# Optimization experiments

Hardware: AMD Instinct MI355X
Metric: run time of the kernel (lower is better)

## Reference

```python
import jax, jax.numpy as jnp
import numpy as np

NHEADS = 16
DIM = 1024


def setup_inputs() -> dict:
    key = jax.random.key(0)
    k1, k2, k3 = jax.random.split(key, 3)
    B, S, D = 4, 2048, DIM
    x = jax.random.normal(k1, (B, S, D), dtype=jnp.float32)
    W_qkv = jax.random.normal(k2, (D, 3 * D), dtype=jnp.float32) * (1.0 / np.sqrt(D))
    b_qkv = jax.random.normal(k3, (3 * D,), dtype=jnp.float32) * 0.01
    return {"x": x, "W_qkv": W_qkv, "b_qkv": b_qkv}


def reference(x, W_qkv, b_qkv):
    B, S, D = x.shape
    H = NHEADS
    Dh = D // H
    qkv = x @ W_qkv + b_qkv                      # [B, S, 3D]
    q, k, v = jnp.split(qkv, 3, axis=-1)         # each [B, S, D]
    # [B, S, H, Dh] -> [B, H, S, Dh]
    q = q.reshape(B, S, H, Dh).transpose(0, 2, 1, 3)
    k = k.reshape(B, S, H, Dh).transpose(0, 2, 1, 3)
    v = v.reshape(B, S, H, Dh).transpose(0, 2, 1, 3)
    scale = 1.0 / np.sqrt(Dh).astype(np.float32)
    scores = jnp.einsum('bhqd,bhkd->bhqk', q, k) * scale
    attn = jax.nn.softmax(scores, axis=-1)
    out = jnp.einsum('bhqk,bhkd->bhqd', attn, v)  # [B, H, S, Dh]
    # FAITHFUL to original: raw view [B,H,S,Dh] -> [B, S, H*Dh] (no transpose back)
    return out.reshape(B, S, H * Dh)
```

## Files before the change

### kernel.cpp

```cpp
#include <hip/hip_runtime.h>
#include <hip/hip_bf16.h>
#include <stdint.h>

typedef float          f32x4 __attribute__((ext_vector_type(4)));
typedef short          s16x8 __attribute__((ext_vector_type(8)));
typedef short          s16x4 __attribute__((ext_vector_type(4)));
typedef unsigned short u16;
typedef u16            u16x4 __attribute__((ext_vector_type(4)));
typedef u16            u16x8 __attribute__((ext_vector_type(8)));

#define DMODEL 1024
#define NH     16
#define DH     64
#define SEQ    2048
#define BATCH  4
#define NROW   (BATCH*SEQ)
#define N3     (3*DMODEL)

#define KEXP 0.1803368801f

__device__ __forceinline__ u16 f2bf(float f) {
    __hip_bfloat16 h = __float2bfloat16(f);
    u16 u;
    __builtin_memcpy(&u, &h, 2);
    return u;
}

typedef const __attribute__((address_space(1))) void* gas_t;
typedef __attribute__((address_space(3))) void* las_t;
__device__ __forceinline__ void async16(void* lds, const void* g) {
    __builtin_amdgcn_global_load_lds((gas_t)g, (las_t)lds, 16, 0, 0);
}

__device__ __forceinline__ f32x4 mfma16(s16x8 a, s16x8 b, f32x4 c) {
    return __builtin_amdgcn_mfma_f32_16x16x32_bf16(a, b, c, 0, 0, 0);
}

#if !defined(__HIP_DEVICE_COMPILE__)
__device__ __forceinline__ f32x4 mfma16k16(s16x4 a, s16x4 b, f32x4 c) {
    (void)a; (void)b; return c;
}
#elif __has_builtin(__builtin_amdgcn_mfma_f32_16x16x16bf16_1k)
__device__ __forceinline__ f32x4 mfma16k16(s16x4 a, s16x4 b, f32x4 c) {
    return __builtin_amdgcn_mfma_f32_16x16x16bf16_1k(a, b, c, 0, 0, 0);
}
#elif __has_builtin(__builtin_amdgcn_mfma_f32_16x16x16_bf16)
__device__ __forceinline__ f32x4 mfma16k16(s16x4 a, s16x4 b, f32x4 c) {
    return __builtin_amdgcn_mfma_f32_16x16x16_bf16(a, b, c, 0, 0, 0);
}
#else
#error "no 16x16x16 bf16 mfma builtin on device"
#endif

__global__ __launch_bounds__(256)
void cast_fused_kernel(const float* __restrict__ xin, u16* __restrict__ xb,
                       const float* __restrict__ W,  u16* __restrict__ Wt)
{
    __shared__ u16 T[64][72];
    const int t = threadIdx.x;
    if (blockIdx.x < 4096) {
        const int i = blockIdx.x * 256 + t;
        const f32x4* p = (const f32x4*)xin;
        f32x4 a = p[2*i], b = p[2*i+1];
        u16x8 o;
        o[0]=f2bf(a[0]); o[1]=f2bf(a[1]); o[2]=f2bf(a[2]); o[3]=f2bf(a[3]);
        o[4]=f2bf(b[0]); o[5]=f2bf(b[1]); o[6]=f2bf(b[2]); o[7]=f2bf(b[3]);
        ((u16x8*)xb)[i] = o;
        return;
    }
    const int bid2 = blockIdx.x - 4096;
    const int n0 = (bid2 % (N3/64)) * 64;
    const int k0 = (bid2 / (N3/64)) * 64;
    {
        const int c4 = t & 15, rr = t >> 4;
        #pragma unroll
        for (int ri = 0; ri < 4; ++ri) {
            const int r = ri*16 + rr;
            f32x4 v = *(const f32x4*)&W[(size_t)(k0 + r) * N3 + n0 + c4*4];
            #pragma unroll
            for (int e = 0; e < 4; ++e) T[r][c4*4+e] = f2bf(v[e]);
        }
    }
    __syncthreads();
    {
        const int nr = t >> 2, kq = t & 3;
        #pragma unroll
        for (int pp = 0; pp < 2; ++pp) {
            const int kb = kq + pp*4;
            u16x8 o;
            #pragma unroll
            for (int e = 0; e < 8; ++e) o[e] = T[kb*8+e][nr];
            *(u16x8*)&Wt[(size_t)(n0 + nr) * DMODEL + k0 + kb*8] = o;
        }
    }
}

__global__ __launch_bounds__(256)
void qkv_mfma_kernel(const u16* __restrict__ xb, const u16* __restrict__ Wt,
                     const float* __restrict__ bias,
                     u16* __restrict__ Qb, u16* __restrict__ Kb, u16* __restrict__ Vt)
{
    __shared__ u16 As[128*32];
    __shared__ u16 Bs[128*32];

    const int tid  = threadIdx.x;
    const int lane = tid & 63;
    const int w    = tid >> 6;
    const int wm   = w >> 1, wn = w & 1;
    const int n0   = blockIdx.x * 128;
    const int m0   = blockIdx.y * 128;

    const int srow = w*32 + (lane >> 2);
    const int scol = (lane & 3) * 8;
    u16* ad0 = &As[(w*2+0)*512 + lane*8];
    u16* ad1 = &As[(w*2+1)*512 + lane*8];
    u16* bd0 = &Bs[(w*2+0)*512 + lane*8];
    u16* bd1 = &Bs[(w*2+1)*512 + lane*8];
    const u16* ag0 = &xb[(size_t)(m0 + srow)      * DMODEL + scol];
    const u16* ag1 = &xb[(size_t)(m0 + srow + 16) * DMODEL + scol];
    const u16* bg0 = &Wt[(size_t)(n0 + srow)      * DMODEL + scol];
    const u16* bg1 = &Wt[(size_t)(n0 + srow + 16) * DMODEL + scol];

    f32x4 acc[4][4];
    #pragma unroll
    for (int i = 0; i < 4; ++i)
        #pragma unroll
        for (int j = 0; j < 4; ++j)
            acc[i][j] = (f32x4){0.f, 0.f, 0.f, 0.f};

    for (int k0 = 0; k0 < DMODEL; k0 += 32) {
        async16(ad0, ag0 + k0);
        async16(ad1, ag1 + k0);
        async16(bd0, bg0 + k0);
        async16(bd1, bg1 + k0);
        __syncthreads();
        s16x8 af[4], bf[4];
        #pragma unroll
        for (int mi = 0; mi < 4; ++mi)
            af[mi] = *(const s16x8*)&As[(wm*64 + mi*16 + (lane&15))*32 + (lane>>4)*8];
        #pragma unroll
        for (int ni = 0; ni < 4; ++ni)
            bf[ni] = *(const s16x8*)&Bs[(wn*64 + ni*16 + (lane&15))*32 + (lane>>4)*8];
        #pragma unroll
        for (int mi = 0; mi < 4; ++mi)
            #pragma unroll
            for (int ni = 0; ni < 4; ++ni)
                acc[mi][ni] = mfma16(af[mi], bf[ni], acc[mi][ni]);
        __syncthreads();
    }

    const int part  = n0 >> 10;
    const int col_l = lane & 15;
    const int h     = ((n0 & 1023) >> 6) + wn;
    float bv[4];
    #pragma unroll
    for (int ni = 0; ni < 4; ++ni) bv[ni] = bias[n0 + wn*64 + ni*16 + col_l];

    const int rbase = m0 + wm*64 + (lane>>4)*4;
    u16* qk = (part == 0) ? Qb : Kb;
    #pragma unroll
    for (int mi = 0; mi < 4; ++mi) {
        const int r0 = rbase + mi*16;
        const int b  = r0 >> 11;
        const int s  = r0 & 2047;
        #pragma unroll
        for (int ni = 0; ni < 4; ++ni) {
            const int d = ni*16 + col_l;
            if (part < 2) {
                u16* base = &qk[(((size_t)b*NH + h)*SEQ + s)*DH + d];
                #pragma unroll
                for (int j = 0; j < 4; ++j) {
                    float v = acc[mi][ni][j] + bv[ni];
                    if (part == 0) v *= KEXP;
                    base[(size_t)j*DH] = f2bf(v);
                }
            } else {
                u16x4 o;
                #pragma unroll
                for (int j = 0; j < 4; ++j) o[j] = f2bf(acc[mi][ni][j] + bv[ni]);
                *(u16x4*)&Vt[(((size_t)b*NH + h)*DH + d)*SEQ + s] = o;
            }
        }
    }
}

__global__ __launch_bounds__(512)
void attn_mfma_kernel(const u16* __restrict__ Qb, const u16* __restrict__ Kb,
                      const u16* __restrict__ Vt, float* __restrict__ out)
{
    __shared__ u16 Ks[2][2][64*64];
    __shared__ u16 Vs[2][2][64*64];

    const int tid  = threadIdx.x;
    const int lane = tid & 63;
    const int w    = tid >> 6;
    const int q0   = blockIdx.x * 256;
    const int bh   = blockIdx.y;
    const size_t qkoff = (size_t)bh * SEQ * DH;

    const int lrow = lane >> 4;
    const int lcol = lane & 15;

    s16x8 qf[2][2];
    #pragma unroll
    for (int mi = 0; mi < 2; ++mi) {
        const u16* qp = &Qb[qkoff + (size_t)(q0 + w*32 + mi*16 + lcol)*DH + lrow*8];
        qf[mi][0] = *(const s16x8*)(qp);
        qf[mi][1] = *(const s16x8*)(qp + 32);
    }

    const int skey = tid >> 3;
    const int sg   = tid & 7;
    const int gsw8 = (sg ^ (skey & 7)) * 8;
    const int sdo  = tid * 8;
    const u16* kgb = &Kb[qkoff + (size_t)skey * DH + gsw8];
    const u16* vgb = &Vt[((size_t)bh * DH + skey) * SEQ + gsw8];

    f32x4 oacc[2][4];
    #pragma unroll
    for (int mi = 0; mi < 2; ++mi)
        #pragma unroll
        for (int nd = 0; nd < 4; ++nd) oacc[mi][nd] = (f32x4){0.f,0.f,0.f,0.f};
    float psum[2] = {0.f, 0.f};

#define STAGE(buf, kb2) do {                                          \
        const size_t _o = (size_t)(kb2) * 128;                        \
        async16(&Ks[buf][0][sdo], kgb + (_o     ) * DH);              \
        async16(&Ks[buf][1][sdo], kgb + (_o + 64) * DH);              \
        async16(&Vs[buf][0][sdo], vgb + _o);                          \
        async16(&Vs[buf][1][sdo], vgb + _o + 64);                     \
    } while (0)

#define COMPUTE(buf, sub) do {                                                   \
        const char* ksb = (const char*)Ks[buf][sub];                             \
        const char* vsb = (const char*)Vs[buf][sub];                             \
        f32x4 sacc[2][4];                                                        \
        _Pragma("unroll")                                                        \
        for (int mi = 0; mi < 2; ++mi)                                           \
            _Pragma("unroll")                                                    \
            for (int ni = 0; ni < 4; ++ni) sacc[mi][ni] = (f32x4){0.f,0.f,0.f,0.f}; \
        _Pragma("unroll")                                                        \
        for (int ni = 0; ni < 4; ++ni) {                                         \
            const int key  = ni*16 + lcol;                                       \
            const int rowb = key * 128;                                          \
            _Pragma("unroll")                                                    \
            for (int ks = 0; ks < 2; ++ks) {                                     \
                const int cb = (ks*64 + lrow*16) ^ ((key & 7) << 4);             \
                s16x8 kf = *(const s16x8*)(ksb + rowb + cb);                     \
                _Pragma("unroll")                                                \
                for (int mi = 0; mi < 2; ++mi)                                   \
                    sacc[mi][ni] = mfma16(kf, qf[mi][ks], sacc[mi][ni]);         \
            }                                                                    \
        }                                                                        \
                \
        s16x4 pa[2][4];                                                          \
        _Pragma("unroll")                                                        \
        for (int mi = 0; mi < 2; ++mi) {                                         \
            float rs = 0.f;                                                      \
            _Pragma("unroll")                                                    \
            for (int ni = 0; ni < 4; ++ni) {                                     \
                u16x4 pk;                                                        \
                _Pragma("unroll")                                                \
                for (int jj = 0; jj < 4; ++jj) {                                 \
                    const float p = __builtin_amdgcn_exp2f(sacc[mi][ni][jj]);    \
                    rs += p;                                                     \
                    pk[jj] = f2bf(p);                                            \
                }                                                                \
                pa[mi][ni] = (s16x4)pk;                                          \
            }                                                                    \
            psum[mi] += rs;                                                      \
        }                                                                        \
                \
        _Pragma("unroll")                                                        \
        for (int ni = 0; ni < 4; ++ni) {                                         \
            _Pragma("unroll")                                                    \
            for (int nd = 0; nd < 4; ++nd) {                                     \
                const int d    = nd*16 + lcol;                                   \
                const int gran = ni*2 + (lrow >> 1);                             \
                const int vb   = d*128 + ((gran ^ (d & 7)) << 4) + (lrow & 1)*8; \
                s16x4 vf = *(const s16x4*)(vsb + vb);                            \
                _Pragma("unroll")                                                \
                for (int mi = 0; mi < 2; ++mi)                                   \
                    oacc[mi][nd] = mfma16k16(pa[mi][ni], vf, oacc[mi][nd]);      \
            }                                                                    \
        }                                                                        \
    } while (0)

    STAGE(0, 0);
    asm volatile("s_waitcnt vmcnt(0)" ::: "memory");
    __builtin_amdgcn_s_barrier();

    for (int kb2 = 0; kb2 < SEQ/128; kb2 += 2) {
        STAGE(1, kb2 + 1);
        COMPUTE(0, 0);
        COMPUTE(0, 1);
        asm volatile("s_waitcnt vmcnt(0)" ::: "memory");
        __builtin_amdgcn_s_barrier();
        if (kb2 + 2 < SEQ/128) STAGE(0, kb2 + 2);
        COMPUTE(1, 0);
        COMPUTE(1, 1);
        asm volatile("s_waitcnt vmcnt(0)" ::: "memory");
        __builtin_amdgcn_s_barrier();
    }

#undef STAGE
#undef COMPUTE

    float* op = out + qkoff;
    #pragma unroll
    for (int mi = 0; mi < 2; ++mi) {
        float l = psum[mi];
        l += __shfl_xor(l, 16);
        l += __shfl_xor(l, 32);
        #pragma unroll
        for (int jj = 0; jj < 4; ++jj) {
            const float rinv = 1.0f / __shfl(l, lrow*4 + jj);
            const int q = q0 + w*32 + mi*16 + lrow*4 + jj;
            #pragma unroll
            for (int nd = 0; nd < 4; ++nd)
                op[(size_t)q*DH + nd*16 + lcol] = oacc[mi][nd][jj] * rinv;
        }
    }
}

extern "C" void kernel_launch(void* const* d_in, const int* in_sizes, int n_in,
                              void* d_out, int out_size, void* d_ws, size_t ws_size,
                              hipStream_t stream)
{
    const float* x    = (const float*)d_in[0];
    const float* W    = (const float*)d_in[1];
    const float* bias = (const float*)d_in[2];
    float* out = (float*)d_out;

    u16* xb = (u16*)d_ws;
    u16* Wt = xb + (size_t)NROW * DMODEL;
    u16* Qb = Wt + (size_t)N3 * DMODEL;
    u16* Kb = Qb + (size_t)BATCH*NH*SEQ*DH;
    u16* Vt = Kb + (size_t)BATCH*NH*SEQ*DH;

    cast_fused_kernel<<<4096 + 768, 256, 0, stream>>>(x, xb, W, Wt);
    qkv_mfma_kernel<<<dim3(N3/128, NROW/128), 256, 0, stream>>>(xb, Wt, bias, Qb, Kb, Vt);
    attn_mfma_kernel<<<dim3(SEQ/256, BATCH*NH), 512, 0, stream>>>(Qb, Kb, Vt, out);
}
```

Measured before the change: 172.7 us.

## Switch attention kernel to 32x32x16 bf16 MFMA tiles

Rewrites the attention inner loop to use 32x32x16 bf16 MFMA for both QK^T and PV, replacing 16x16x32 and 16x16x16 instructions. Each wave now handles 32 queries as a single M tile, with cross-half lane shuffles to rearrange the exponentiated probabilities into the A-operand layout for the PV product. The aim is fewer MFMA issues and LDS fragment reads per tile and a larger K per instruction. The cost is extra shuffles per block, larger accumulator register tiles, and a new output-store mapping.

Measured after the change: 171.7 us. About the same (-0.5%).

```diff
diff --git a/kernel.cpp b/kernel.cpp
--- a/kernel.cpp
+++ b/kernel.cpp
@@ -2,12 +2,14 @@
 #include <hip/hip_bf16.h>
 #include <stdint.h>
 
-typedef float          f32x4 __attribute__((ext_vector_type(4)));
-typedef short          s16x8 __attribute__((ext_vector_type(8)));
-typedef short          s16x4 __attribute__((ext_vector_type(4)));
+typedef float          f32x4  __attribute__((ext_vector_type(4)));
+typedef float          f32x16 __attribute__((ext_vector_type(16)));
+typedef short          s16x8  __attribute__((ext_vector_type(8)));
 typedef unsigned short u16;
 typedef u16            u16x4 __attribute__((ext_vector_type(4)));
 typedef u16            u16x8 __attribute__((ext_vector_type(8)));
+typedef unsigned int   u32;
+typedef u32            u32x4 __attribute__((ext_vector_type(4)));
 
 #define DMODEL 1024
 #define NH     16
@@ -35,22 +37,9 @@
 __device__ __forceinline__ f32x4 mfma16(s16x8 a, s16x8 b, f32x4 c) {
     return __builtin_amdgcn_mfma_f32_16x16x32_bf16(a, b, c, 0, 0, 0);
 }
-
-#if !defined(__HIP_DEVICE_COMPILE__)
-__device__ __forceinline__ f32x4 mfma16k16(s16x4 a, s16x4 b, f32x4 c) {
-    (void)a; (void)b; return c;
-}
-#elif __has_builtin(__builtin_amdgcn_mfma_f32_16x16x16bf16_1k)
-__device__ __forceinline__ f32x4 mfma16k16(s16x4 a, s16x4 b, f32x4 c) {
-    return __builtin_amdgcn_mfma_f32_16x16x16bf16_1k(a, b, c, 0, 0, 0);
-}
-#elif __has_builtin(__builtin_amdgcn_mfma_f32_16x16x16_bf16)
-__device__ __forceinline__ f32x4 mfma16k16(s16x4 a, s16x4 b, f32x4 c) {
-    return __builtin_amdgcn_mfma_f32_16x16x16_bf16(a, b, c, 0, 0, 0);
-}
-#else
-#error "no 16x16x16 bf16 mfma builtin on device"
-#endif
+__device__ __forceinline__ f32x16 mfma32(s16x8 a, s16x8 b, f32x16 c) {
+    return __builtin_amdgcn_mfma_f32_32x32x16_bf16(a, b, c, 0, 0, 0);
+}
 
 __global__ __launch_bounds__(256)
 void cast_fused_kernel(const float* __restrict__ xin, u16* __restrict__ xb,
@@ -198,15 +187,15 @@
     const int bh   = blockIdx.y;
     const size_t qkoff = (size_t)bh * SEQ * DH;
 
-    const int lrow = lane >> 4;
-    const int lcol = lane & 15;
-
-    s16x8 qf[2][2];
-    #pragma unroll
-    for (int mi = 0; mi < 2; ++mi) {
-        const u16* qp = &Qb[qkoff + (size_t)(q0 + w*32 + mi*16 + lcol)*DH + lrow*8];
-        qf[mi][0] = *(const s16x8*)(qp);
-        qf[mi][1] = *(const s16x8*)(qp + 32);
+    const int l5  = lane >> 5;
+    const int l31 = lane & 31;
+
+    s16x8 qf[4];
+    {
+        const u16* qp = &Qb[qkoff + (size_t)(q0 + w*32 + l31)*DH];
+        #pragma unroll
+        for (int dop = 0; dop < 4; ++dop)
+            qf[dop] = *(const s16x8*)(qp + dop*16 + l5*8);
     }
 
     const int skey = tid >> 3;
@@ -216,12 +205,10 @@
     const u16* kgb = &Kb[qkoff + (size_t)skey * DH + gsw8];
     const u16* vgb = &Vt[((size_t)bh * DH + skey) * SEQ + gsw8];
 
-    f32x4 oacc[2][4];
-    #pragma unroll
-    for (int mi = 0; mi < 2; ++mi)
-        #pragma unroll
-        for (int nd = 0; nd < 4; ++nd) oacc[mi][nd] = (f32x4){0.f,0.f,0.f,0.f};
-    float psum[2] = {0.f, 0.f};
+    f32x16 oacc[2];
+    #pragma unroll
+    for (int i = 0; i < 16; ++i) { oacc[0][i] = 0.f; oacc[1][i] = 0.f; }
+    float psum = 0.f;
 
 #define STAGE(buf, kb2) do {                                          \
         const size_t _o = (size_t)(kb2) * 128;                        \
@@ -234,54 +221,60 @@
 #define COMPUTE(buf, sub) do {                                                   \
         const char* ksb = (const char*)Ks[buf][sub];                             \
         const char* vsb = (const char*)Vs[buf][sub];                             \
-        f32x4 sacc[2][4];                                                        \
+        f32x16 sacc[2];                                                          \
         _Pragma("unroll")                                                        \
-        for (int mi = 0; mi < 2; ++mi)                                           \
+        for (int i = 0; i < 16; ++i) { sacc[0][i] = 0.f; sacc[1][i] = 0.f; }     \
+        _Pragma("unroll")                                                        \
+        for (int dop = 0; dop < 4; ++dop) {                                      \
             _Pragma("unroll")                                                    \
-            for (int ni = 0; ni < 4; ++ni) sacc[mi][ni] = (f32x4){0.f,0.f,0.f,0.f}; \
-        _Pragma("unroll")                                                        \
-        for (int ni = 0; ni < 4; ++ni) {                                         \
-            const int key  = ni*16 + lcol;                                       \
-            const int rowb = key * 128;                                          \
-            _Pragma("unroll")                                                    \
-            for (int ks = 0; ks < 2; ++ks) {                                     \
-                const int cb = (ks*64 + lrow*16) ^ ((key & 7) << 4);             \
-                s16x8 kf = *(const s16x8*)(ksb + rowb + cb);                     \
-                _Pragma("unroll")                                                \
-                for (int mi = 0; mi < 2; ++mi)                                   \
-                    sacc[mi][ni] = mfma16(kf, qf[mi][ks], sacc[mi][ni]);         \
+            for (int kb32 = 0; kb32 < 2; ++kb32) {                               \
+                const int rowK = kb32*32 + l31;                                  \
+                const int gK   = 2*dop + l5;                                     \
+                s16x8 kf = *(const s16x8*)(ksb + rowK*128                        \
+                                           + ((gK ^ (rowK & 7)) << 4));          \
+                sacc[kb32] = mfma32(kf, qf[dop], sacc[kb32]);                    \
             }                                                                    \
         }                                                                        \
-                \
-        s16x4 pa[2][4];                                                          \
+            \
+                                      \
+        u32 pk2[2][8];                                                           \
+        float rs = 0.f;                                                          \
         _Pragma("unroll")                                                        \
-        for (int mi = 0; mi < 2; ++mi) {                                         \
-            float rs = 0.f;                                                      \
+        for (int kb32 = 0; kb32 < 2; ++kb32) {                                   \
             _Pragma("unroll")                                                    \
-            for (int ni = 0; ni < 4; ++ni) {                                     \
-                u16x4 pk;                                                        \
-                _Pragma("unroll")                                                \
-                for (int jj = 0; jj < 4; ++jj) {                                 \
-                    const float p = __builtin_amdgcn_exp2f(sacc[mi][ni][jj]);    \
-                    rs += p;                                                     \
-                    pk[jj] = f2bf(p);                                            \
-                }                                                                \
-                pa[mi][ni] = (s16x4)pk;                                          \
+            for (int pj = 0; pj < 8; ++pj) {                                     \
+                const int r0 = 4*(pj>>1) + 2*(pj&1);                             \
+                const float p0 = __builtin_amdgcn_exp2f(sacc[kb32][r0]);         \
+                const float p1 = __builtin_amdgcn_exp2f(sacc[kb32][r0+1]);       \
+                rs += p0 + p1;                                                   \
+                pk2[kb32][pj] = (u32)f2bf(p0) | ((u32)f2bf(p1) << 16);           \
             }                                                                    \
-            psum[mi] += rs;                                                      \
         }                                                                        \
-                \
+        psum += rs;                                                              \
+              \
+                    \
         _Pragma("unroll")                                                        \
-        for (int ni = 0; ni < 4; ++ni) {                                         \
+        for (int kop = 0; kop < 4; ++kop) {                                      \
+            const int kb = kop >> 1;                                             \
+            const int k2 = (kop & 1) * 4;                                        \
+            const u32 s0 = l5 ? pk2[kb][k2+0] : pk2[kb][k2+2];                   \
+            const u32 s1 = l5 ? pk2[kb][k2+1] : pk2[kb][k2+3];                   \
+            const u32 f0 = __shfl_xor(s0, 32);                                   \
+            const u32 f1 = __shfl_xor(s1, 32);                                   \
+            u32x4 pw;                                                            \
+            pw[0] = l5 ? f0 : pk2[kb][k2+0];                                     \
+            pw[1] = l5 ? f1 : pk2[kb][k2+1];                                     \
+            pw[2] = l5 ? pk2[kb][k2+2] : f0;                                     \
+            pw[3] = l5 ? pk2[kb][k2+3] : f1;                                     \
+            s16x8 paf;                                                           \
+            __builtin_memcpy(&paf, &pw, 16);                                     \
             _Pragma("unroll")                                                    \
-            for (int nd = 0; nd < 4; ++nd) {                                     \
-                const int d    = nd*16 + lcol;                                   \
-                const int gran = ni*2 + (lrow >> 1);                             \
-                const int vb   = d*128 + ((gran ^ (d & 7)) << 4) + (lrow & 1)*8; \
-                s16x4 vf = *(const s16x4*)(vsb + vb);                            \
-                _Pragma("unroll")                                                \
-                for (int mi = 0; mi < 2; ++mi)                                   \
-                    oacc[mi][nd] = mfma16k16(pa[mi][ni], vf, oacc[mi][nd]);      \
+            for (int ndblk = 0; ndblk < 2; ++ndblk) {                            \
+                const int rowV = ndblk*32 + l31;                                 \
+                const int gV   = 2*kop + l5;                                     \
+                s16x8 vf = *(const s16x8*)(vsb + rowV*128                        \
+                                           + ((gV ^ (rowV & 7)) << 4));          \
+                oacc[ndblk] = mfma32(paf, vf, oacc[ndblk]);                      \
             }                                                                    \
         }                                                                        \
     } while (0)
@@ -306,20 +299,16 @@
 #undef STAGE
 #undef COMPUTE
 
+    const float pt = psum + __shfl_xor(psum, 32);
+    const float rinv_own = 1.0f / pt;
     float* op = out + qkoff;
     #pragma unroll
-    for (int mi = 0; mi < 2; ++mi) {
-        float l = psum[mi];
-        l += __shfl_xor(l, 16);
-        l += __shfl_xor(l, 32);
-        #pragma unroll
-        for (int jj = 0; jj < 4; ++jj) {
-            const float rinv = 1.0f / __shfl(l, lrow*4 + jj);
-            const int q = q0 + w*32 + mi*16 + lrow*4 + jj;
-            #pragma unroll
-            for (int nd = 0; nd < 4; ++nd)
-                op[(size_t)q*DH + nd*16 + lcol] = oacc[mi][nd][jj] * rinv;
-        }
+    for (int r = 0; r < 16; ++r) {
+        const int qrow = (r & 3) + 8*(r >> 2) + 4*l5;
+        const float ri = __shfl(rinv_own, qrow);
+        const size_t q = (size_t)(q0 + w*32 + qrow);
+        op[q*DH + l31]      = oacc[0][r] * ri;
+        op[q*DH + 32 + l31] = oacc[1][r] * ri;
     }
 }
 
```
